# Optimization experiments

Measured on AMD Instinct MI355X. Metric: run time of the kernel, lower is better.

Reference implementation:

```python
import jax, jax.numpy as jnp
import numpy as np

N_NODES = 50000
N_EDGES = 1600000
IN_CH = 512
OUT_CH = 64
ITERATIONS = 3


def _spmm(adj_index, adj_values, x):
    # sparse @ dense: out[r] = sum_{e: row[e]==r} vals[e] * x[col[e]]
    row, col = adj_index[0], adj_index[1]
    gathered = adj_values[:, None] * x[col]  # [E, F]
    return jax.ops.segment_sum(gathered, row, num_segments=x.shape[0])


def setup_inputs() -> dict:
    key = jax.random.key(0)
    k1, k2, k3, k4, k5 = jax.random.split(key, 5)
    adj_index = jax.random.randint(k1, (2, N_EDGES), 0, N_NODES, dtype=jnp.int64)
    # positive normalized-like edge weights ~ 1/avg_degree
    adj_values = jax.random.uniform(k2, (N_EDGES,), dtype=jnp.float32) / 32.0
    features = jax.random.normal(k3, (N_NODES, IN_CH), dtype=jnp.float32)
    xavier_w = float(np.sqrt(6.0 / (IN_CH + OUT_CH)))
    weight_matrix = jax.random.uniform(k4, (IN_CH, OUT_CH), dtype=jnp.float32, minval=-xavier_w, maxval=xavier_w)
    xavier_b = float(np.sqrt(6.0 / (1 + OUT_CH)))
    bias = jax.random.uniform(k5, (1, OUT_CH), dtype=jnp.float32, minval=-xavier_b, maxval=xavier_b)
    return {"adj_index": adj_index, "adj_values": adj_values, "features": features,
            "weight_matrix": weight_matrix, "bias": bias}


def reference(adj_index, adj_values, features, weight_matrix, bias):
    # dense projection (dropout_rate=0.0 / eval mode -> identity dropout)
    base = features @ weight_matrix  # [N, OUT_CH]
    # repeated sparse-dense propagation: A^(iterations-1) @ (X W)
    for _ in range(ITERATIONS - 1):
        base = _spmm(adj_index, adj_values, base)
    return base + bias
```

## Files before the change

kernel.cpp:

```cpp
#include <hip/hip_runtime.h>
#include <hip/hip_bf16.h>

typedef __attribute__((ext_vector_type(8))) __bf16 bf16x8;
typedef __attribute__((ext_vector_type(4))) float f32x4;

#define IN_CH 512
#define OUT_CH 64
#define BS 98
#define NB 512
#define CHUNK 4096
#define CAP 4096

__device__ inline unsigned short f2bf(float f) {
    __hip_bfloat16 h = __float2bfloat16(f);
    return __builtin_bit_cast(unsigned short, h);
}
__device__ inline float bf2f(unsigned short u) {
    return __uint_as_float(((unsigned)u) << 16);
}

__global__ __launch_bounds__(512) void prep_kernel(
    const float* __restrict__ W, __hip_bfloat16* __restrict__ Wf,
    int* __restrict__ bcur)
{
    const int t = blockIdx.x * 512 + threadIdx.x;
    if (t < NB) bcur[t] = t * CAP;
    const int ct = t >> 10;
    const int rem = t & 1023;
    const int ks = rem >> 6;
    const int l = rem & 63;
    const int col = ct * 16 + (l & 15);
    const int kb = ks * 32 + (l >> 4) * 8;
    __hip_bfloat16* dst = Wf + (size_t)t * 8;
    #pragma unroll
    for (int j = 0; j < 8; ++j)
        dst[j] = (__hip_bfloat16)W[(size_t)(kb + j) * OUT_CH + col];
}

__global__ __launch_bounds__(512, 4) void gemmscatter_kernel(
    const int* __restrict__ rows, const int* __restrict__ cols,
    const float* __restrict__ vals, int* __restrict__ bcur,
    unsigned* __restrict__ segc, unsigned char* __restrict__ segr, int E,
    int nScatter,
    const float* __restrict__ A, const bf16x8* __restrict__ wf,
    __hip_bfloat16* __restrict__ outb, int N)
{
    __shared__ __align__(16) char smem[36 * 1024];
    const int tid = threadIdx.x;

    if (blockIdx.x < nScatter) {
        unsigned*       c_lds = (unsigned*)smem;
        unsigned char*  r_lds = (unsigned char*)(smem + 16384);
        unsigned short* b_lds = (unsigned short*)(smem + 20480);
        int* hist    = (int*)(smem + 28672);
        int* scn     = (int*)(smem + 30720);
        int* lbase   = (int*)(smem + 32768);
        int* runBase = (int*)(smem + 34816);

        const int c0 = blockIdx.x * CHUNK;
        const int cnt = min(CHUNK, E - c0);
        const int base = c0 + tid * 8;

        hist[tid] = 0;
        __syncthreads();

        int myb[8]; unsigned myc[8]; unsigned char myr[8];
        int nmine = 0;
        if (base + 8 <= E) {
            nmine = 8;
            int4 r4[2], c4[2]; float4 v4[2];
            #pragma unroll
            for (int q = 0; q < 2; ++q) {
                r4[q] = *(const int4*)(rows + base + q * 4);
                c4[q] = *(const int4*)(cols + base + q * 4);
                v4[q] = *(const float4*)(vals + base + q * 4);
            }
            #pragma unroll
            for (int q = 0; q < 2; ++q) {
                int rr[4] = {r4[q].x, r4[q].y, r4[q].z, r4[q].w};
                int cc[4] = {c4[q].x, c4[q].y, c4[q].z, c4[q].w};
                float vv[4] = {v4[q].x, v4[q].y, v4[q].z, v4[q].w};
                #pragma unroll
                for (int u = 0; u < 4; ++u) {
                    int j = q * 4 + u;
                    int r = rr[u];
                    int b = r / BS;
                    myb[j] = b;
                    myr[j] = (unsigned char)(r - b * BS);
                    myc[j] = ((unsigned)cc[u] << 16) | f2bf(vv[u]);
                    atomicAdd(&hist[b], 1);
                }
            }
        } else {
            #pragma unroll 1
            for (int j = 0; j < 8; ++j) {
                int e = base + j;
                if (e < E) {
                    int r = rows[e];
                    int b = r / BS;
                    myb[j] = b;
                    myr[j] = (unsigned char)(r - b * BS);
                    myc[j] = ((unsigned)cols[e] << 16) | f2bf(vals[e]);
                    atomicAdd(&hist[b], 1);
                    nmine = j + 1;
                }
            }
        }
        __syncthreads();

        {
            int h = hist[tid];
            scn[tid] = h;
            __syncthreads();
            for (int ofs = 1; ofs < NB; ofs <<= 1) {
                int u = 0;
                if (tid >= ofs) u = scn[tid - ofs];
                __syncthreads();
                if (tid >= ofs) scn[tid] += u;
                __syncthreads();
            }
            int excl = scn[tid] - h;
            lbase[tid] = excl;
            hist[tid] = excl;
            runBase[tid] = h ? atomicAdd(&bcur[tid], h) : 0;
        }
        __syncthreads();

        #pragma unroll 1
        for (int j = 0; j < nmine; ++j) {
            int pos = atomicAdd(&hist[myb[j]], 1);
            c_lds[pos] = myc[j];
            r_lds[pos] = myr[j];
            b_lds[pos] = (unsigned short)myb[j];
        }
        __syncthreads();

        for (int idx = tid; idx < cnt; idx += 512) {
            int b = b_lds[idx];
            int gpos = runBase[b] + (idx - lbase[b]);
            segc[gpos] = c_lds[idx];
            segr[gpos] = r_lds[idx];
        }
    } else {
        char* Abf = smem;
        const int row0 = (blockIdx.x - nScatter) * 32;

        float4 v[8];
        #pragma unroll
        for (int j = 0; j < 8; ++j) {
            int f = j * 512 + tid;
            int row = f >> 7, c4 = f & 127;
            int rg = row0 + row; rg = rg < N ? rg : N - 1;
            v[j] = *(const float4*)(A + (size_t)rg * IN_CH + c4 * 4);
        }
        #pragma unroll
        for (int j = 0; j < 8; ++j) {
            int f = j * 512 + tid;
            int row = f >> 7, c4 = f & 127;
            int blk = c4 >> 1, half = c4 & 1;
            ushort4 h;
            h.x = f2bf(v[j].x); h.y = f2bf(v[j].y);
            h.z = f2bf(v[j].z); h.w = f2bf(v[j].w);
            *(ushort4*)(Abf + row * 1024 + ((blk ^ (row & 7)) << 4) + (half << 3)) = h;
        }
        __syncthreads();

        const int lane = tid & 63;
        const int wave = tid >> 6;
        const int rowblk = wave & 1;
        const int ct = wave >> 1;
        const int arow = rowblk * 16 + (lane & 15);
        const int kgb = lane >> 4;

        bf16x8 a[16];
        #pragma unroll
        for (int ks = 0; ks < 16; ++ks)
            a[ks] = *(const bf16x8*)(Abf + arow * 1024 +
                                     (((ks * 4 + kgb) ^ (arow & 7)) << 4));

        f32x4 acc = {0.f, 0.f, 0.f, 0.f};
        #pragma unroll
        for (int ks = 0; ks < 16; ++ks)
            acc = __builtin_amdgcn_mfma_f32_16x16x32_bf16(
                a[ks], wf[(ct * 16 + ks) * 64 + lane], acc, 0, 0, 0);

        const int col = ct * 16 + (lane & 15);
        const int rr = row0 + rowblk * 16 + (lane >> 4) * 4;
        #pragma unroll
        for (int i = 0; i < 4; ++i) {
            int r = rr + i;
            if (r < N)
                outb[(size_t)r * OUT_CH + col] = __float2bfloat16(acc[i]);
        }
    }
}

__global__ __launch_bounds__(512) void sortspmm_kernel(
    const int* __restrict__ bcur,
    unsigned* __restrict__ segc, const unsigned char* __restrict__ segr,
    int* __restrict__ offs, int* __restrict__ rend,
    const __hip_bfloat16* __restrict__ x,
    __hip_bfloat16* __restrict__ y1, int N)
{
    __shared__ unsigned sorted4[CAP];
    __shared__ int hist[BS + 1];
    __shared__ int cursor[BS];

    const int b = blockIdx.x;
    const int t = threadIdx.x;
    const int s = b * CAP;
    const int cnt = bcur[b] - s;

    if (t < BS + 1) hist[t] = 0;
    __syncthreads();

    unsigned ek[8]; unsigned char er[8];
    #pragma unroll
    for (int j = 0; j < 8; ++j) {
        int idx = t + j * 512;
        if (idx < cnt) {
            ek[j] = segc[s + idx];
            er[j] = segr[s + idx];
            atomicAdd(&hist[er[j]], 1);
        }
    }
    __syncthreads();

    if (t == 0) {
        int run = 0;
        for (int i = 0; i < BS; ++i) { int c = hist[i]; hist[i] = run; run += c; }
        hist[BS] = run;
    }
    __syncthreads();

    if (t < BS) {
        cursor[t] = hist[t];
        offs[b * BS + t] = s + hist[t];
        rend[b * BS + t] = s + hist[t + 1];
    }
    __syncthreads();

    #pragma unroll
    for (int j = 0; j < 8; ++j) {
        int idx = t + j * 512;
        if (idx < cnt) {
            int pos = atomicAdd(&cursor[er[j]], 1);
            sorted4[pos] = ek[j];
        }
    }
    __syncthreads();

    #pragma unroll
    for (int j = 0; j < 8; ++j) {
        int idx = t + j * 512;
        if (idx < cnt) segc[s + idx] = sorted4[idx];
    }

    const int lane = t & 63;
    const int wave = t >> 6;
    const int grp = lane >> 4;
    const int l16 = lane & 15;
    const ushort* xp = (const ushort*)x + l16 * 4;

    #pragma unroll 1
    for (int sweep = 0; sweep < 4; ++sweep) {
        int rr = sweep * 32 + wave * 4 + grp;
        int rrc = rr < BS ? rr : BS - 1;
        int rs = hist[rrc];
        int re = hist[rrc + 1];
        int gr = b * BS + rr;
        if (rr >= BS || gr >= N) re = rs;

        float4 acc = {0.f, 0.f, 0.f, 0.f};
        for (int i0 = rs; i0 < re; i0 += 16) {
            unsigned p[16];
            #pragma unroll
            for (int j = 0; j < 16; ++j) {
                int idx = i0 + j;
                p[j] = sorted4[idx < re ? idx : rs];
            }
            ushort4 xv[16];
            #pragma unroll
            for (int j = 0; j < 16; ++j)
                xv[j] = *(const ushort4*)(xp + (size_t)(p[j] >> 16) * OUT_CH);
            #pragma unroll
            for (int j = 0; j < 16; ++j) {
                float wv = (i0 + j < re) ? __uint_as_float(p[j] << 16) : 0.f;
                acc.x = fmaf(wv, bf2f(xv[j].x), acc.x);
                acc.y = fmaf(wv, bf2f(xv[j].y), acc.y);
                acc.z = fmaf(wv, bf2f(xv[j].z), acc.z);
                acc.w = fmaf(wv, bf2f(xv[j].w), acc.w);
            }
        }
        if (rr < BS && gr < N) {
            ushort4 h;
            h.x = f2bf(acc.x); h.y = f2bf(acc.y);
            h.z = f2bf(acc.z); h.w = f2bf(acc.w);
            *(ushort4*)((ushort*)y1 + (size_t)gr * OUT_CH + l16 * 4) = h;
        }
    }
}

__global__ __launch_bounds__(256) void spmm_row_kernel(
    const int* __restrict__ offs, const int* __restrict__ rend,
    const unsigned* __restrict__ segc,
    const __hip_bfloat16* __restrict__ x,
    float* __restrict__ yf, const float* __restrict__ bias, int N)
{
    const int tid = threadIdx.x;
    const int lane = tid & 63;
    const int wave = tid >> 6;
    const int grp = lane >> 4;
    const int l16 = lane & 15;

    int r = (blockIdx.x * 4 + wave) * 4 + grp;
    const bool rv = r < N;
    const int rc = rv ? r : N - 1;
    const int s = offs[rc];
    const int e = rv ? rend[rc] : s;

    int m = e - s;
    m = max(m, __shfl_xor(m, 16));
    m = max(m, __shfl_xor(m, 32));
    const int iters = (m + 15) >> 4;

    const ushort* xp = (const ushort*)x + l16 * 4;

    float4 acc = {0.f, 0.f, 0.f, 0.f};
    for (int it = 0; it < iters; ++it) {
        const int base = s + it * 16;
        unsigned p[16];
        #pragma unroll
        for (int j = 0; j < 16; ++j) {
            int idx = base + j;
            p[j] = segc[idx < e ? idx : s];
        }
        ushort4 xv[16];
        #pragma unroll
        for (int j = 0; j < 16; ++j)
            xv[j] = *(const ushort4*)(xp + (size_t)(p[j] >> 16) * OUT_CH);
        #pragma unroll
        for (int j = 0; j < 16; ++j) {
            int idx = base + j;
            float wv = (idx < e) ? __uint_as_float(p[j] << 16) : 0.f;
            acc.x = fmaf(wv, bf2f(xv[j].x), acc.x);
            acc.y = fmaf(wv, bf2f(xv[j].y), acc.y);
            acc.z = fmaf(wv, bf2f(xv[j].z), acc.z);
            acc.w = fmaf(wv, bf2f(xv[j].w), acc.w);
        }
    }

    if (rv) {
        float4 bv = *(const float4*)(bias + l16 * 4);
        float4 o;
        o.x = acc.x + bv.x; o.y = acc.y + bv.y;
        o.z = acc.z + bv.z; o.w = acc.w + bv.w;
        *(float4*)(yf + (size_t)r * OUT_CH + l16 * 4) = o;
    }
}

static inline size_t align_up(size_t v) { return (v + 255) & ~(size_t)255; }

extern "C" void kernel_launch(void* const* d_in, const int* in_sizes, int n_in,
                              void* d_out, int out_size, void* d_ws, size_t ws_size,
                              hipStream_t stream)
{
    const int*   adj  = (const int*)d_in[0];
    const float* vals = (const float*)d_in[1];
    const float* feat = (const float*)d_in[2];
    const float* Wm   = (const float*)d_in[3];
    const float* bias = (const float*)d_in[4];

    const int E = in_sizes[1];
    const int N = in_sizes[2] / IN_CH;
    const int* rows  = adj;
    const int* colsI = adj + E;

    char* w = (char*)d_ws;
    size_t o = 0;
    __hip_bfloat16* B0b = (__hip_bfloat16*)(w + o); o += align_up((size_t)N * OUT_CH * 2);
    __hip_bfloat16* Y1b = (__hip_bfloat16*)(w + o); o += align_up((size_t)N * OUT_CH * 2);
    __hip_bfloat16* Wf  = (__hip_bfloat16*)(w + o); o += align_up((size_t)IN_CH * OUT_CH * 2);
    int*           bcur = (int*)          (w + o); o += align_up(NB * sizeof(int));
    int*           offs = (int*)          (w + o); o += align_up((size_t)NB * BS * sizeof(int));
    int*           rend = (int*)          (w + o); o += align_up((size_t)NB * BS * sizeof(int));
    unsigned*      segc = (unsigned*)     (w + o); o += align_up((size_t)NB * CAP * sizeof(unsigned));
    unsigned char* segr = (unsigned char*)(w + o); o += align_up((size_t)NB * CAP);
    (void)ws_size; (void)n_in; (void)out_size;

    prep_kernel<<<8, 512, 0, stream>>>(Wm, Wf, bcur);

    const int nScatter = (E + CHUNK - 1) / CHUNK;
    const int nGemm = (N + 31) / 32;
    gemmscatter_kernel<<<nScatter + nGemm, 512, 0, stream>>>(
        rows, colsI, vals, bcur, segc, segr, E, nScatter,
        feat, (const bf16x8*)Wf, B0b, N);

    sortspmm_kernel<<<NB, 512, 0, stream>>>(
        bcur, segc, segr, offs, rend, B0b, Y1b, N);

    spmm_row_kernel<<<(N + 15) / 16, 256, 0, stream>>>(
        offs, rend, segc, Y1b, (float*)d_out, bias, N);
}
```

Before: 101.1 us.

## Re-sort per-block edges in both SpMM passes instead of storing sorted CSR

Both propagation passes now use one templated kernel that rebuilds the per-row sorted edge list in shared memory from the bucketed segments. This removes the global write-back of the sorted edges and the offs/rend arrays, and the second pass reads its edges from LDS instead of global memory. Each pass also now splits the 64 output channels into two halves of 32, with 16 lanes each loading 2 channels. That gives smaller gathers per lane but walks the edge list twice. The cost is a second histogram and shared-memory sort, and only 512 blocks in the final pass instead of about 3125 smaller ones.

Result: slower. 114.6 us (+13.4%).

```diff
diff --git a/kernel.cpp b/kernel.cpp
--- a/kernel.cpp
+++ b/kernel.cpp
@@ -195,12 +195,14 @@
     }
 }
 
-__global__ __launch_bounds__(512) void sortspmm_kernel(
+template<int FINAL>
+__global__ __launch_bounds__(512) void pass_kernel(
     const int* __restrict__ bcur,
-    unsigned* __restrict__ segc, const unsigned char* __restrict__ segr,
-    int* __restrict__ offs, int* __restrict__ rend,
+    const unsigned* __restrict__ segc, const unsigned char* __restrict__ segr,
     const __hip_bfloat16* __restrict__ x,
-    __hip_bfloat16* __restrict__ y1, int N)
+    __hip_bfloat16* __restrict__ yb,
+    float* __restrict__ yf,
+    const float* __restrict__ bias, int N)
 {
     __shared__ unsigned sorted4[CAP];
     __shared__ int hist[BS + 1];
@@ -233,11 +235,7 @@
     }
     __syncthreads();
 
-    if (t < BS) {
-        cursor[t] = hist[t];
-        offs[b * BS + t] = s + hist[t];
-        rend[b * BS + t] = s + hist[t + 1];
-    }
+    if (t < BS) cursor[t] = hist[t];
     __syncthreads();
 
     #pragma unroll
@@ -250,112 +248,53 @@
     }
     __syncthreads();
 
-    #pragma unroll
-    for (int j = 0; j < 8; ++j) {
-        int idx = t + j * 512;
-        if (idx < cnt) segc[s + idx] = sorted4[idx];
-    }
-
     const int lane = t & 63;
     const int wave = t >> 6;
     const int grp = lane >> 4;
     const int l16 = lane & 15;
-    const ushort* xp = (const ushort*)x + l16 * 4;
 
     #pragma unroll 1
-    for (int sweep = 0; sweep < 4; ++sweep) {
-        int rr = sweep * 32 + wave * 4 + grp;
-        int rrc = rr < BS ? rr : BS - 1;
-        int rs = hist[rrc];
-        int re = hist[rrc + 1];
-        int gr = b * BS + rr;
-        if (rr >= BS || gr >= N) re = rs;
-
-        float4 acc = {0.f, 0.f, 0.f, 0.f};
-        for (int i0 = rs; i0 < re; i0 += 16) {
-            unsigned p[16];
-            #pragma unroll
-            for (int j = 0; j < 16; ++j) {
-                int idx = i0 + j;
-                p[j] = sorted4[idx < re ? idx : rs];
-            }
-            ushort4 xv[16];
-            #pragma unroll
-            for (int j = 0; j < 16; ++j)
-                xv[j] = *(const ushort4*)(xp + (size_t)(p[j] >> 16) * OUT_CH);
-            #pragma unroll
-            for (int j = 0; j < 16; ++j) {
-                float wv = (i0 + j < re) ? __uint_as_float(p[j] << 16) : 0.f;
-                acc.x = fmaf(wv, bf2f(xv[j].x), acc.x);
-                acc.y = fmaf(wv, bf2f(xv[j].y), acc.y);
-                acc.z = fmaf(wv, bf2f(xv[j].z), acc.z);
-                acc.w = fmaf(wv, bf2f(xv[j].w), acc.w);
-            }
-        }
-        if (rr < BS && gr < N) {
-            ushort4 h;
-            h.x = f2bf(acc.x); h.y = f2bf(acc.y);
-            h.z = f2bf(acc.z); h.w = f2bf(acc.w);
-            *(ushort4*)((ushort*)y1 + (size_t)gr * OUT_CH + l16 * 4) = h;
-        }
-    }
-}
-
-__global__ __launch_bounds__(256) void spmm_row_kernel(
-    const int* __restrict__ offs, const int* __restrict__ rend,
-    const unsigned* __restrict__ segc,
-    const __hip_bfloat16* __restrict__ x,
-    float* __restrict__ yf, const float* __restrict__ bias, int N)
-{
-    const int tid = threadIdx.x;
-    const int lane = tid & 63;
-    const int wave = tid >> 6;
-    const int grp = lane >> 4;
-    const int l16 = lane & 15;
-
-    int r = (blockIdx.x * 4 + wave) * 4 + grp;
-    const bool rv = r < N;
-    const int rc = rv ? r : N - 1;
-    const int s = offs[rc];
-    const int e = rv ? rend[rc] : s;
-
-    int m = e - s;
-    m = max(m, __shfl_xor(m, 16));
-    m = max(m, __shfl_xor(m, 32));
-    const int iters = (m + 15) >> 4;
-
-    const ushort* xp = (const ushort*)x + l16 * 4;
-
-    float4 acc = {0.f, 0.f, 0.f, 0.f};
-    for (int it = 0; it < iters; ++it) {
-        const int base = s + it * 16;
-        unsigned p[16];
-        #pragma unroll
-        for (int j = 0; j < 16; ++j) {
-            int idx = base + j;
-            p[j] = segc[idx < e ? idx : s];
-        }
-        ushort4 xv[16];
-        #pragma unroll
-        for (int j = 0; j < 16; ++j)
-            xv[j] = *(const ushort4*)(xp + (size_t)(p[j] >> 16) * OUT_CH);
-        #pragma unroll
-        for (int j = 0; j < 16; ++j) {
-            int idx = base + j;
-            float wv = (idx < e) ? __uint_as_float(p[j] << 16) : 0.f;
-            acc.x = fmaf(wv, bf2f(xv[j].x), acc.x);
-            acc.y = fmaf(wv, bf2f(xv[j].y), acc.y);
-            acc.z = fmaf(wv, bf2f(xv[j].z), acc.z);
-            acc.w = fmaf(wv, bf2f(xv[j].w), acc.w);
-        }
-    }
-
-    if (rv) {
-        float4 bv = *(const float4*)(bias + l16 * 4);
-        float4 o;
-        o.x = acc.x + bv.x; o.y = acc.y + bv.y;
-        o.z = acc.z + bv.z; o.w = acc.w + bv.w;
-        *(float4*)(yf + (size_t)r * OUT_CH + l16 * 4) = o;
+    for (int h = 0; h < 2; ++h) {
+        const ushort* xp = (const ushort*)x + h * 32 + l16 * 2;
+        #pragma unroll 1
+        for (int sweep = 0; sweep < 4; ++sweep) {
+            int rr = sweep * 32 + wave * 4 + grp;
+            int rrc = rr < BS ? rr : BS - 1;
+            int rs = hist[rrc];
+            int re = hist[rrc + 1];
+            int gr = b * BS + rr;
+            if (rr >= BS || gr >= N) re = rs;
+
+            float2 acc = {0.f, 0.f};
+            for (int i0 = rs; i0 < re; i0 += 16) {
+                unsigned p[16];
+                #pragma unroll
+                for (int j = 0; j < 16; ++j) {
+                    int idx = i0 + j;
+                    p[j] = sorted4[idx < re ? idx : rs];
+                }
+                ushort2 xv[16];
+                #pragma unroll
+                for (int j = 0; j < 16; ++j)
+                    xv[j] = *(const ushort2*)(xp + (size_t)(p[j] >> 16) * OUT_CH);
+                #pragma unroll
+                for (int j = 0; j < 16; ++j) {
+                    float wv = (i0 + j < re) ? __uint_as_float(p[j] << 16) : 0.f;
+                    acc.x = fmaf(wv, bf2f(xv[j].x), acc.x);
+                    acc.y = fmaf(wv, bf2f(xv[j].y), acc.y);
+                }
+            }
+            if (rr < BS && gr < N) {
+                if (FINAL) {
+                    float2 bv = *(const float2*)(bias + h * 32 + l16 * 2);
+                    float2 o; o.x = acc.x + bv.x; o.y = acc.y + bv.y;
+                    *(float2*)(yf + (size_t)gr * OUT_CH + h * 32 + l16 * 2) = o;
+                } else {
+                    ushort2 o; o.x = f2bf(acc.x); o.y = f2bf(acc.y);
+                    *(ushort2*)((ushort*)yb + (size_t)gr * OUT_CH + h * 32 + l16 * 2) = o;
+                }
+            }
+        }
     }
 }
 
@@ -382,8 +321,6 @@
     __hip_bfloat16* Y1b = (__hip_bfloat16*)(w + o); o += align_up((size_t)N * OUT_CH * 2);
     __hip_bfloat16* Wf  = (__hip_bfloat16*)(w + o); o += align_up((size_t)IN_CH * OUT_CH * 2);
     int*           bcur = (int*)          (w + o); o += align_up(NB * sizeof(int));
-    int*           offs = (int*)          (w + o); o += align_up((size_t)NB * BS * sizeof(int));
-    int*           rend = (int*)          (w + o); o += align_up((size_t)NB * BS * sizeof(int));
     unsigned*      segc = (unsigned*)     (w + o); o += align_up((size_t)NB * CAP * sizeof(unsigned));
     unsigned char* segr = (unsigned char*)(w + o); o += align_up((size_t)NB * CAP);
     (void)ws_size; (void)n_in; (void)out_size;
@@ -396,9 +333,9 @@
         rows, colsI, vals, bcur, segc, segr, E, nScatter,
         feat, (const bf16x8*)Wf, B0b, N);
 
-    sortspmm_kernel<<<NB, 512, 0, stream>>>(
-        bcur, segc, segr, offs, rend, B0b, Y1b, N);
-
-    spmm_row_kernel<<<(N + 15) / 16, 256, 0, stream>>>(
-        offs, rend, segc, Y1b, (float*)d_out, bias, N);
-}
+    pass_kernel<0><<<NB, 512, 0, stream>>>(
+        bcur, segc, segr, B0b, Y1b, nullptr, nullptr, N);
+
+    pass_kernel<1><<<NB, 512, 0, stream>>>(
+        bcur, segc, segr, Y1b, nullptr, (float*)d_out, bias, N);
+}
```
